# Kernel tuning notes

Hardware: AMD Instinct MI355X
Metric: run time of the kernel (lower is better)

Reference implementation:

```python
import jax, jax.numpy as jnp
import numpy as np

NUM_NODES = 200000
NUM_EDGES = 640000
RANK = 16
EMBED_DIM = 128


def setup_inputs() -> dict:
    key = jax.random.key(0)
    k1, k2, k3 = jax.random.split(key, 3)
    U = jax.random.normal(k1, (NUM_NODES, RANK), dtype=jnp.float32)
    V = jax.random.normal(k2, (RANK, EMBED_DIM), dtype=jnp.float32)
    edge_index = jax.random.randint(k3, (2, NUM_EDGES), 0, NUM_NODES, dtype=jnp.int64)
    return {"U": U, "V": V, "edge_index": edge_index}


def reference(U, V, edge_index):
    # Low-rank projection: [N, r] @ [r, d] -> [N, d]
    embeddings = jnp.matmul(U, V)
    src, dst = edge_index[0], edge_index[1]
    # Mean aggregation (PyG MessagePassing aggr='mean', source_to_target):
    # gather messages from source nodes, segment-mean into destination nodes.
    msgs = embeddings[src]  # [E, d]
    summed = jax.ops.segment_sum(msgs, dst, num_segments=NUM_NODES)  # [N, d]
    counts = jax.ops.segment_sum(jnp.ones((edge_index.shape[1],), dtype=embeddings.dtype),
                                 dst, num_segments=NUM_NODES)  # [N]
    denom = jnp.maximum(counts, 1.0)  # isolated nodes -> 0 output (scatter-mean semantics)
    return summed / denom[:, None]
```

## Files before the change

kernel.cpp:

```cpp
#include <hip/hip_runtime.h>
#include <hip/hip_bf16.h>

#define RANK 16
#define EMBED_DIM 128

__global__ void detect_idx_dtype(const unsigned int* __restrict__ words,
                                 int nwords, int* __restrict__ flag) {
    unsigned int v = 0;
    for (int i = threadIdx.x; i < 2048; i += 256) {
        int w = 2 * i + 1;
        if (w < nwords) v |= words[w];
    }
    if (__any(v != 0)) {
        if ((threadIdx.x & 63) == 0) atomicOr(flag, 1);
    }
}

__global__ void scatter_rank(const float* __restrict__ U,
                             const void* __restrict__ edge_index,
                             float* __restrict__ Usum,
                             float* __restrict__ counts,
                             const int* __restrict__ flag,
                             int E) {
    int gid = blockIdx.x * 256 + threadIdx.x;
    int e = gid >> 4;
    int j = gid & 15;
    if (e >= E) return;
    int src, dst;
    if (*flag) {
        const int* ei = (const int*)edge_index;
        src = ei[e];
        dst = ei[E + e];
    } else {
        const int* ei = (const int*)edge_index;
        src = ei[2 * e];
        dst = ei[2 * (E + e)];
    }
    atomicAdd(&Usum[(size_t)dst * RANK + j], U[(size_t)src * RANK + j]);
    if (j == 0) atomicAdd(&counts[dst], 1.0f);
}

__global__ __launch_bounds__(256) void project_out(
        const float* __restrict__ Usum,
        const float* __restrict__ counts,
        const float* __restrict__ V,
        float* __restrict__ out) {
    __shared__ float4 Vs4[RANK * EMBED_DIM / 4];
    int t = threadIdx.x;
    const float4* V4 = (const float4*)V;
    Vs4[t] = V4[t];
    Vs4[t + 256] = V4[t + 256];
    __syncthreads();

    int q = t & 31;
    int w = t >> 5;
    int n0 = blockIdx.x * 32 + 4 * w;

    const float4* Us4 = (const float4*)Usum;
    float4 a[4][4];
#pragma unroll
    for (int r = 0; r < 4; ++r)
#pragma unroll
        for (int k4 = 0; k4 < 4; ++k4)
            a[r][k4] = Us4[(size_t)(n0 + r) * 4 + k4];

    float4 acc[4];
#pragma unroll
    for (int r = 0; r < 4; ++r) acc[r] = make_float4(0.f, 0.f, 0.f, 0.f);

#pragma unroll
    for (int k = 0; k < RANK; ++k) {
        float4 v = Vs4[k * 32 + q];
#pragma unroll
        for (int r = 0; r < 4; ++r) {
            float ar = (k & 3) == 0 ? a[r][k >> 2].x
                     : (k & 3) == 1 ? a[r][k >> 2].y
                     : (k & 3) == 2 ? a[r][k >> 2].z
                                    : a[r][k >> 2].w;
            acc[r].x = fmaf(ar, v.x, acc[r].x);
            acc[r].y = fmaf(ar, v.y, acc[r].y);
            acc[r].z = fmaf(ar, v.z, acc[r].z);
            acc[r].w = fmaf(ar, v.w, acc[r].w);
        }
    }

    float4* out4 = (float4*)out;
#pragma unroll
    for (int r = 0; r < 4; ++r) {
        float c = counts[n0 + r];
        float s = 1.0f / fmaxf(c, 1.0f);
        out4[(size_t)(n0 + r) * (EMBED_DIM / 4) + q] =
            make_float4(acc[r].x * s, acc[r].y * s, acc[r].z * s, acc[r].w * s);
    }
}

extern "C" void kernel_launch(void* const* d_in, const int* in_sizes, int n_in,
                              void* d_out, int out_size, void* d_ws, size_t ws_size,
                              hipStream_t stream) {
    const float* U = (const float*)d_in[0];
    const float* V = (const float*)d_in[1];
    const void* EI = d_in[2];
    float* out = (float*)d_out;

    const int N = in_sizes[0] / RANK;
    const int E = in_sizes[2] / 2;

    float* Usum = (float*)d_ws;
    float* counts = Usum + (size_t)N * RANK;
    int* flag = (int*)(counts + N);
    size_t zero_bytes = ((size_t)N * RANK + N + 1) * sizeof(float);

    hipMemsetAsync(d_ws, 0, zero_bytes, stream);

    detect_idx_dtype<<<1, 256, 0, stream>>>((const unsigned int*)EI,
                                            in_sizes[2], flag);

    int scatter_threads = E * RANK;
    scatter_rank<<<(scatter_threads + 255) / 256, 256, 0, stream>>>(
        U, EI, Usum, counts, flag, E);

    project_out<<<N / 32, 256, 0, stream>>>(Usum, counts, V, out);
}
```

Measured before the change: 200.2 us.

## Replace atomic scatter with CSR build and per-node gather-then-project

```diff
diff --git a/kernel.cpp b/kernel.cpp
--- a/kernel.cpp
+++ b/kernel.cpp
@@ -3,6 +3,7 @@
 
 #define RANK 16
 #define EMBED_DIM 128
+
 
 __global__ void detect_idx_dtype(const unsigned int* __restrict__ words,
                                  int nwords, int* __restrict__ flag) {
@@ -16,81 +17,124 @@
     }
 }
 
-__global__ void scatter_rank(const float* __restrict__ U,
-                             const void* __restrict__ edge_index,
-                             float* __restrict__ Usum,
-                             float* __restrict__ counts,
-                             const int* __restrict__ flag,
-                             int E) {
-    int gid = blockIdx.x * 256 + threadIdx.x;
-    int e = gid >> 4;
-    int j = gid & 15;
+__global__ void hist_kernel(const void* __restrict__ ei,
+                            const int* __restrict__ flag,
+                            unsigned* __restrict__ counts, int E) {
+    int e = blockIdx.x * 256 + threadIdx.x;
+    if (e >= E) return;
+    int dst;
+    if (*flag) dst = ((const int*)ei)[E + e];
+    else       dst = ((const int*)ei)[2 * (E + e)];
+    atomicAdd(&counts[dst], 1u);
+}
+
+__global__ void scan1(const unsigned* __restrict__ counts,
+                      unsigned* __restrict__ offsets,
+                      unsigned* __restrict__ partials, int N) {
+    __shared__ unsigned s[256];
+    int t = threadIdx.x;
+    int i = blockIdx.x * 256 + t;
+    unsigned v = (i < N) ? counts[i] : 0u;
+    s[t] = v; __syncthreads();
+    for (int off = 1; off < 256; off <<= 1) {
+        unsigned x = (t >= off) ? s[t - off] : 0u;
+        __syncthreads();
+        s[t] += x; __syncthreads();
+    }
+    if (i < N) offsets[i] = s[t] - v;
+    if (t == 255) partials[blockIdx.x] = s[255];
+}
+
+__global__ void scan2(unsigned* __restrict__ partials, int P) {
+    __shared__ unsigned s[1024];
+    int t = threadIdx.x;
+    unsigned v = (t < P) ? partials[t] : 0u;
+    s[t] = v; __syncthreads();
+    for (int off = 1; off < 1024; off <<= 1) {
+        unsigned x = (t >= off) ? s[t - off] : 0u;
+        __syncthreads();
+        s[t] += x; __syncthreads();
+    }
+    if (t < P) partials[t] = s[t] - v;
+}
+
+__global__ void scan3(unsigned* __restrict__ offsets,
+                      unsigned* __restrict__ cursors,
+                      const unsigned* __restrict__ partials, int N) {
+    int i = blockIdx.x * 256 + threadIdx.x;
+    if (i >= N) return;
+    unsigned o = offsets[i] + partials[blockIdx.x];
+    offsets[i] = o;
+    cursors[i] = o;
+}
+
+__global__ void fill_kernel(const void* __restrict__ ei,
+                            const int* __restrict__ flag,
+                            unsigned* __restrict__ cursors,
+                            unsigned* __restrict__ csr_src, int E) {
+    int e = blockIdx.x * 256 + threadIdx.x;
     if (e >= E) return;
     int src, dst;
-    if (*flag) {
-        const int* ei = (const int*)edge_index;
-        src = ei[e];
-        dst = ei[E + e];
-    } else {
-        const int* ei = (const int*)edge_index;
-        src = ei[2 * e];
-        dst = ei[2 * (E + e)];
-    }
-    atomicAdd(&Usum[(size_t)dst * RANK + j], U[(size_t)src * RANK + j]);
-    if (j == 0) atomicAdd(&counts[dst], 1.0f);
+    if (*flag) { const int* p = (const int*)ei; src = p[e];     dst = p[E + e]; }
+    else       { const int* p = (const int*)ei; src = p[2 * e]; dst = p[2 * (E + e)]; }
+    unsigned pos = atomicAdd(&cursors[dst], 1u);
+    csr_src[pos] = (unsigned)src;
 }
 
-__global__ __launch_bounds__(256) void project_out(
-        const float* __restrict__ Usum,
-        const float* __restrict__ counts,
-        const float* __restrict__ V,
-        float* __restrict__ out) {
+__global__ __launch_bounds__(256) void gather_project(
+        const float* __restrict__ U, const float* __restrict__ V,
+        const unsigned* __restrict__ counts,
+        const unsigned* __restrict__ offsets,
+        const unsigned* __restrict__ csr_src,
+        float* __restrict__ out, int N) {
     __shared__ float4 Vs4[RANK * EMBED_DIM / 4];
+    __shared__ float usum[32][RANK + 1];
     int t = threadIdx.x;
     const float4* V4 = (const float4*)V;
     Vs4[t] = V4[t];
     Vs4[t + 256] = V4[t + 256];
+
+    int g = t >> 4, lane = t & 15;
+    for (int rep = 0; rep < 2; ++rep) {
+        int ln = rep * 16 + g;
+        int n = blockIdx.x * 32 + ln;
+        float acc = 0.f;
+        if (n < N) {
+            unsigned start = offsets[n];
+            unsigned deg = counts[n];
+            for (unsigned k = 0; k < deg; ++k) {
+                unsigned src = csr_src[start + k];
+                acc += U[(size_t)src * RANK + lane];
+            }
+        }
+        usum[ln][lane] = acc;
+    }
     __syncthreads();
 
-    int q = t & 31;
-    int w = t >> 5;
-    int n0 = blockIdx.x * 32 + 4 * w;
-
-    const float4* Us4 = (const float4*)Usum;
-    float4 a[4][4];
+    int ln = t >> 3;
+    int c8 = t & 7;
+    int n = blockIdx.x * 32 + ln;
+    if (n >= N) return;
+    float a[RANK];
 #pragma unroll
-    for (int r = 0; r < 4; ++r)
-#pragma unroll
-        for (int k4 = 0; k4 < 4; ++k4)
-            a[r][k4] = Us4[(size_t)(n0 + r) * 4 + k4];
-
-    float4 acc[4];
-#pragma unroll
-    for (int r = 0; r < 4; ++r) acc[r] = make_float4(0.f, 0.f, 0.f, 0.f);
-
-#pragma unroll
-    for (int k = 0; k < RANK; ++k) {
-        float4 v = Vs4[k * 32 + q];
-#pragma unroll
-        for (int r = 0; r < 4; ++r) {
-            float ar = (k & 3) == 0 ? a[r][k >> 2].x
-                     : (k & 3) == 1 ? a[r][k >> 2].y
-                     : (k & 3) == 2 ? a[r][k >> 2].z
-                                    : a[r][k >> 2].w;
-            acc[r].x = fmaf(ar, v.x, acc[r].x);
-            acc[r].y = fmaf(ar, v.y, acc[r].y);
-            acc[r].z = fmaf(ar, v.z, acc[r].z);
-            acc[r].w = fmaf(ar, v.w, acc[r].w);
-        }
-    }
-
+    for (int k = 0; k < RANK; ++k) a[k] = usum[ln][k];
+    float deg = (float)counts[n];
+    float scale = 1.0f / fmaxf(deg, 1.0f);
     float4* out4 = (float4*)out;
 #pragma unroll
-    for (int r = 0; r < 4; ++r) {
-        float c = counts[n0 + r];
-        float s = 1.0f / fmaxf(c, 1.0f);
-        out4[(size_t)(n0 + r) * (EMBED_DIM / 4) + q] =
-            make_float4(acc[r].x * s, acc[r].y * s, acc[r].z * s, acc[r].w * s);
+    for (int s = 0; s < 4; ++s) {
+        int c4 = c8 + 8 * s;
+        float4 acc = make_float4(0.f, 0.f, 0.f, 0.f);
+#pragma unroll
+        for (int k = 0; k < RANK; ++k) {
+            float4 v = Vs4[k * 32 + c4];
+            acc.x = fmaf(a[k], v.x, acc.x);
+            acc.y = fmaf(a[k], v.y, acc.y);
+            acc.z = fmaf(a[k], v.z, acc.z);
+            acc.w = fmaf(a[k], v.w, acc.w);
+        }
+        out4[(size_t)n * (EMBED_DIM / 4) + c4] =
+            make_float4(acc.x * scale, acc.y * scale, acc.z * scale, acc.w * scale);
     }
 }
 
@@ -105,19 +149,26 @@
     const int N = in_sizes[0] / RANK;
     const int E = in_sizes[2] / 2;
 
-    float* Usum = (float*)d_ws;
-    float* counts = Usum + (size_t)N * RANK;
-    int* flag = (int*)(counts + N);
-    size_t zero_bytes = ((size_t)N * RANK + N + 1) * sizeof(float);
+    unsigned* ws = (unsigned*)d_ws;
+    int*      flag     = (int*)ws;
+    unsigned* counts   = ws + 1;
+    unsigned* offsets  = counts + N;
+    unsigned* cursors  = offsets + N;
+    unsigned* partials = cursors + N;
+    unsigned* csr_src  = partials + 1024;
 
-    hipMemsetAsync(d_ws, 0, zero_bytes, stream);
+    const int NB = (N + 255) / 256;
+    const int EB = (E + 255) / 256;
+
+    hipMemsetAsync(d_ws, 0, sizeof(unsigned) * (size_t)(N + 1), stream);
 
     detect_idx_dtype<<<1, 256, 0, stream>>>((const unsigned int*)EI,
                                             in_sizes[2], flag);
-
-    int scatter_threads = E * RANK;
-    scatter_rank<<<(scatter_threads + 255) / 256, 256, 0, stream>>>(
-        U, EI, Usum, counts, flag, E);
-
-    project_out<<<N / 32, 256, 0, stream>>>(Usum, counts, V, out);
+    hist_kernel<<<EB, 256, 0, stream>>>(EI, flag, counts, E);
+    scan1<<<NB, 256, 0, stream>>>(counts, offsets, partials, N);
+    scan2<<<1, 1024, 0, stream>>>(partials, NB);
+    scan3<<<NB, 256, 0, stream>>>(offsets, cursors, partials, N);
+    fill_kernel<<<EB, 256, 0, stream>>>(EI, flag, cursors, csr_src, E);
+    gather_project<<<(N + 31) / 32, 256, 0, stream>>>(U, V, counts, offsets,
+                                                      csr_src, out, N);
 }
```

Result: slower. 246.8 us (+23.2%).

## Bin edges by destination block and accumulate in shared memory before projection

Applied to the files above, without the earlier changes.

```diff
diff --git a/kernel.cpp b/kernel.cpp
--- a/kernel.cpp
+++ b/kernel.cpp
@@ -3,94 +3,148 @@
 
 #define RANK 16
 #define EMBED_DIM 128
+#define NODES_PER_BIN 64
 
-__global__ void detect_idx_dtype(const unsigned int* __restrict__ words,
-                                 int nwords, int* __restrict__ flag) {
-    unsigned int v = 0;
-    for (int i = threadIdx.x; i < 2048; i += 256) {
-        int w = 2 * i + 1;
-        if (w < nwords) v |= words[w];
+
+__device__ __forceinline__ bool detect_i32(const unsigned* __restrict__ w,
+                                           int nwords) {
+    unsigned v = 0;
+#pragma unroll
+    for (int r = 0; r < 8; ++r) {
+        int idx = 2 * ((int)(threadIdx.x & 63) + 64 * r) + 1;
+        if (idx < nwords) v |= w[idx];
     }
-    if (__any(v != 0)) {
-        if ((threadIdx.x & 63) == 0) atomicOr(flag, 1);
-    }
+    return __any(v != 0);
 }
 
-__global__ void scatter_rank(const float* __restrict__ U,
-                             const void* __restrict__ edge_index,
-                             float* __restrict__ Usum,
-                             float* __restrict__ counts,
-                             const int* __restrict__ flag,
-                             int E) {
-    int gid = blockIdx.x * 256 + threadIdx.x;
-    int e = gid >> 4;
-    int j = gid & 15;
+__global__ void bin_hist(const unsigned* __restrict__ ei,
+                         unsigned* __restrict__ bin_counts,
+                         int E, int nwords) {
+    bool i32 = detect_i32(ei, nwords);
+    const int* p = (const int*)ei;
+    int e = blockIdx.x * 256 + threadIdx.x;
+    if (e >= E) return;
+    int dst = i32 ? p[E + e] : p[2 * (E + e)];
+    atomicAdd(&bin_counts[dst >> 6], 1u);
+}
+
+__global__ __launch_bounds__(1024) void bin_scan(
+        const unsigned* __restrict__ bin_counts,
+        unsigned* __restrict__ bin_offsets,
+        unsigned* __restrict__ bin_cursors, int nbins) {
+    __shared__ unsigned s[1024];
+    int t = threadIdx.x;
+    unsigned c[4], tsum = 0;
+#pragma unroll
+    for (int i = 0; i < 4; ++i) {
+        int idx = 4 * t + i;
+        c[i] = (idx < nbins) ? bin_counts[idx] : 0u;
+        tsum += c[i];
+    }
+    s[t] = tsum; __syncthreads();
+    for (int off = 1; off < 1024; off <<= 1) {
+        unsigned x = (t >= off) ? s[t - off] : 0u;
+        __syncthreads();
+        s[t] += x; __syncthreads();
+    }
+    unsigned run = s[t] - tsum;
+#pragma unroll
+    for (int i = 0; i < 4; ++i) {
+        int idx = 4 * t + i;
+        if (idx < nbins) { bin_offsets[idx] = run; bin_cursors[idx] = run; }
+        run += c[i];
+    }
+    if (t == 1023) bin_offsets[nbins] = s[1023];
+}
+
+__global__ void bin_fill(const unsigned* __restrict__ ei,
+                         unsigned* __restrict__ bin_cursors,
+                         unsigned* __restrict__ records,
+                         int E, int nwords) {
+    bool i32 = detect_i32(ei, nwords);
+    const int* p = (const int*)ei;
+    int e = blockIdx.x * 256 + threadIdx.x;
     if (e >= E) return;
     int src, dst;
-    if (*flag) {
-        const int* ei = (const int*)edge_index;
-        src = ei[e];
-        dst = ei[E + e];
-    } else {
-        const int* ei = (const int*)edge_index;
-        src = ei[2 * e];
-        dst = ei[2 * (E + e)];
-    }
-    atomicAdd(&Usum[(size_t)dst * RANK + j], U[(size_t)src * RANK + j]);
-    if (j == 0) atomicAdd(&counts[dst], 1.0f);
+    if (i32) { src = p[e];     dst = p[E + e]; }
+    else     { src = p[2 * e]; dst = p[2 * (E + e)]; }
+    unsigned pos = atomicAdd(&bin_cursors[dst >> 6], 1u);
+    records[pos] = ((unsigned)src << 6) | (unsigned)(dst & 63);
 }
 
-__global__ __launch_bounds__(256) void project_out(
-        const float* __restrict__ Usum,
-        const float* __restrict__ counts,
-        const float* __restrict__ V,
-        float* __restrict__ out) {
-    __shared__ float4 Vs4[RANK * EMBED_DIM / 4];
+__global__ __launch_bounds__(256, 4) void accum_project(
+        const float* __restrict__ U, const float* __restrict__ V,
+        const unsigned* __restrict__ bin_offsets,
+        const unsigned* __restrict__ records,
+        float* __restrict__ out, int N) {
+    __shared__ float usum[NODES_PER_BIN * RANK];
+    __shared__ unsigned ucnt[NODES_PER_BIN];
     int t = threadIdx.x;
-    const float4* V4 = (const float4*)V;
-    Vs4[t] = V4[t];
-    Vs4[t + 256] = V4[t + 256];
+    int bin = blockIdx.x;
+    int base = bin * NODES_PER_BIN;
+
+    float4* us4 = (float4*)usum;
+    us4[t] = make_float4(0.f, 0.f, 0.f, 0.f);
+    if (t < NODES_PER_BIN) ucnt[t] = 0u;
     __syncthreads();
 
-    int q = t & 31;
-    int w = t >> 5;
-    int n0 = blockIdx.x * 32 + 4 * w;
+    unsigned start = bin_offsets[bin];
+    unsigned end   = bin_offsets[bin + 1];
+    int g = t >> 4, lane = t & 15;
+    for (unsigned e = start + g; e < end; e += 16) {
+        unsigned rec = records[e];
+        unsigned src = rec >> 6;
+        unsigned d6  = rec & 63u;
+        float val = U[(size_t)src * RANK + lane];
+        atomicAdd(&usum[d6 * RANK + lane], val);
+        if (lane == 0) atomicAdd(&ucnt[d6], 1u);
+    }
+    __syncthreads();
 
-    const float4* Us4 = (const float4*)Usum;
-    float4 a[4][4];
+    int col4 = t & 31;
+    int n0 = (t >> 5) * 8;
+    const float4* V4 = (const float4*)V;
+    float4 acc[8];
 #pragma unroll
-    for (int r = 0; r < 4; ++r)
+    for (int i = 0; i < 8; ++i) acc[i] = make_float4(0.f, 0.f, 0.f, 0.f);
 #pragma unroll
-        for (int k4 = 0; k4 < 4; ++k4)
-            a[r][k4] = Us4[(size_t)(n0 + r) * 4 + k4];
-
-    float4 acc[4];
+    for (int k4 = 0; k4 < 4; ++k4) {
+        float4 v0 = V4[(4 * k4 + 0) * 32 + col4];
+        float4 v1 = V4[(4 * k4 + 1) * 32 + col4];
+        float4 v2 = V4[(4 * k4 + 2) * 32 + col4];
+        float4 v3 = V4[(4 * k4 + 3) * 32 + col4];
 #pragma unroll
-    for (int r = 0; r < 4; ++r) acc[r] = make_float4(0.f, 0.f, 0.f, 0.f);
-
-#pragma unroll
-    for (int k = 0; k < RANK; ++k) {
-        float4 v = Vs4[k * 32 + q];
-#pragma unroll
-        for (int r = 0; r < 4; ++r) {
-            float ar = (k & 3) == 0 ? a[r][k >> 2].x
-                     : (k & 3) == 1 ? a[r][k >> 2].y
-                     : (k & 3) == 2 ? a[r][k >> 2].z
-                                    : a[r][k >> 2].w;
-            acc[r].x = fmaf(ar, v.x, acc[r].x);
-            acc[r].y = fmaf(ar, v.y, acc[r].y);
-            acc[r].z = fmaf(ar, v.z, acc[r].z);
-            acc[r].w = fmaf(ar, v.w, acc[r].w);
+        for (int i = 0; i < 8; ++i) {
+            float4 a = us4[(n0 + i) * 4 + k4];
+            acc[i].x = fmaf(a.x, v0.x, acc[i].x);
+            acc[i].y = fmaf(a.x, v0.y, acc[i].y);
+            acc[i].z = fmaf(a.x, v0.z, acc[i].z);
+            acc[i].w = fmaf(a.x, v0.w, acc[i].w);
+            acc[i].x = fmaf(a.y, v1.x, acc[i].x);
+            acc[i].y = fmaf(a.y, v1.y, acc[i].y);
+            acc[i].z = fmaf(a.y, v1.z, acc[i].z);
+            acc[i].w = fmaf(a.y, v1.w, acc[i].w);
+            acc[i].x = fmaf(a.z, v2.x, acc[i].x);
+            acc[i].y = fmaf(a.z, v2.y, acc[i].y);
+            acc[i].z = fmaf(a.z, v2.z, acc[i].z);
+            acc[i].w = fmaf(a.z, v2.w, acc[i].w);
+            acc[i].x = fmaf(a.w, v3.x, acc[i].x);
+            acc[i].y = fmaf(a.w, v3.y, acc[i].y);
+            acc[i].z = fmaf(a.w, v3.z, acc[i].z);
+            acc[i].w = fmaf(a.w, v3.w, acc[i].w);
         }
     }
 
     float4* out4 = (float4*)out;
 #pragma unroll
-    for (int r = 0; r < 4; ++r) {
-        float c = counts[n0 + r];
-        float s = 1.0f / fmaxf(c, 1.0f);
-        out4[(size_t)(n0 + r) * (EMBED_DIM / 4) + q] =
-            make_float4(acc[r].x * s, acc[r].y * s, acc[r].z * s, acc[r].w * s);
+    for (int i = 0; i < 8; ++i) {
+        int n = base + n0 + i;
+        if (n < N) {
+            float s = 1.0f / fmaxf((float)ucnt[n0 + i], 1.0f);
+            out4[(size_t)n * (EMBED_DIM / 4) + col4] =
+                make_float4(acc[i].x * s, acc[i].y * s,
+                            acc[i].z * s, acc[i].w * s);
+        }
     }
 }
 
@@ -99,25 +153,25 @@
                               hipStream_t stream) {
     const float* U = (const float*)d_in[0];
     const float* V = (const float*)d_in[1];
-    const void* EI = d_in[2];
+    const unsigned* EI = (const unsigned*)d_in[2];
     float* out = (float*)d_out;
 
-    const int N = in_sizes[0] / RANK;
-    const int E = in_sizes[2] / 2;
+    int N = in_sizes[0] / RANK;
+    int E = in_sizes[2] / 2;
+    int nwords = in_sizes[2];
+    int nbins = (N + NODES_PER_BIN - 1) / NODES_PER_BIN;
 
-    float* Usum = (float*)d_ws;
-    float* counts = Usum + (size_t)N * RANK;
-    int* flag = (int*)(counts + N);
-    size_t zero_bytes = ((size_t)N * RANK + N + 1) * sizeof(float);
+    unsigned* ws = (unsigned*)d_ws;
+    unsigned* bin_counts  = ws;
+    unsigned* bin_offsets = bin_counts + nbins;
+    unsigned* bin_cursors = bin_offsets + nbins + 1;
+    unsigned* records     = bin_cursors + nbins;
 
-    hipMemsetAsync(d_ws, 0, zero_bytes, stream);
+    const int EB = (E + 255) / 256;
 
-    detect_idx_dtype<<<1, 256, 0, stream>>>((const unsigned int*)EI,
-                                            in_sizes[2], flag);
-
-    int scatter_threads = E * RANK;
-    scatter_rank<<<(scatter_threads + 255) / 256, 256, 0, stream>>>(
-        U, EI, Usum, counts, flag, E);
-
-    project_out<<<N / 32, 256, 0, stream>>>(Usum, counts, V, out);
+    hipMemsetAsync(bin_counts, 0, sizeof(unsigned) * (size_t)nbins, stream);
+    bin_hist<<<EB, 256, 0, stream>>>(EI, bin_counts, E, nwords);
+    bin_scan<<<1, 1024, 0, stream>>>(bin_counts, bin_offsets, bin_cursors, nbins);
+    bin_fill<<<EB, 256, 0, stream>>>(EI, bin_cursors, records, E, nwords);
+    accum_project<<<nbins, 256, 0, stream>>>(U, V, bin_offsets, records, out, N);
 }
```

Measured after the change: 359.3 us. +79.4%, slower.
